# Optimization experiments

Hardware: AMD Instinct MI355X
Metric: run time of the kernel (lower is better)

## Reference

```python
import jax, jax.numpy as jnp
import numpy as np

B, D, C = 4096, 4096, 1024


def setup_inputs() -> dict:
    key = jax.random.key(0)
    kx, kw = jax.random.split(key)
    x = jax.random.normal(kx, (B, D), dtype=jnp.float32)
    # kaiming_normal_ with nonlinearity='relu': std = sqrt(2 / fan_in)
    W = jax.random.normal(kw, (C, D), dtype=jnp.float32) * jnp.sqrt(2.0 / D)
    return {"x": x, "W": W}


def reference(x, W):
    # Original: -( (x[:, :, None] - W.T[None, :, :])**2 ).mean(axis=1)
    d = x.shape[1]
    x_sq = jnp.sum(x * x, axis=1, keepdims=True)        # [B, 1]
    w_sq = jnp.sum(W * W, axis=1)[None, :]              # [1, C]
    cross = jnp.einsum('bd,cd->bc', x, W)               # [B, C] tensor-core GEMM
    return -(x_sq - 2.0 * cross + w_sq) / d
```

## Files before the change

kernel.cpp:

```cpp
#include <hip/hip_runtime.h>
#include <hip/hip_bf16.h>


typedef float f32x4 __attribute__((ext_vector_type(4)));
typedef float f32x2 __attribute__((ext_vector_type(2)));
typedef float f32x16 __attribute__((ext_vector_type(16)));
typedef int i32x4 __attribute__((ext_vector_type(4)));
typedef int i32x8 __attribute__((ext_vector_type(8)));

#define BDIM 4096
#define DDIM 4096
#define CDIM 1024
#define TM 256
#define TN 256
#define BK 64
#define KSPLIT 4
#define NIT ((DDIM / KSPLIT) / BK)
#define SCALE 32.0f
#define INV_SS (1.0f/1024.0f)
#define PSCALE 0.0625f

#define WAITV(N) asm volatile("s_waitcnt vmcnt(" #N ")" ::: "memory")

__global__ __launch_bounds__(256) void cvt_rowsq(
    const float* __restrict__ x, const float* __restrict__ W,
    unsigned char* __restrict__ xb, unsigned char* __restrict__ wb,
    float* __restrict__ xsq, float* __restrict__ wsq)
{
    const int lane = threadIdx.x & 63;
    const int row = blockIdx.x * 4 + (threadIdx.x >> 6);

    const float* src;
    unsigned char* dst;
    float* sq;
    if (row < BDIM) {
        src = x + (size_t)row * DDIM;
        dst = xb + (size_t)row * DDIM;
        sq = xsq + row;
    } else {
        int r = row - BDIM;
        src = W + (size_t)r * DDIM;
        dst = wb + (size_t)r * DDIM;
        sq = wsq + r;
    }

    const float4* s4 = (const float4*)src;
    unsigned int* d4 = (unsigned int*)dst;
    float a = 0.f;
    #pragma unroll
    for (int s = 0; s < DDIM / 4 / 64; ++s) {
        float4 f = s4[lane + 64 * s];
        a += f.x * f.x + f.y * f.y + f.z * f.z + f.w * f.w;
        unsigned int p = 0;
        p = __builtin_amdgcn_cvt_pk_fp8_f32(f.x * SCALE, f.y * SCALE, p, false);
        p = __builtin_amdgcn_cvt_pk_fp8_f32(f.z * SCALE, f.w * SCALE, p, true);
        d4[lane + 64 * s] = p;
    }
    #pragma unroll
    for (int off = 32; off > 0; off >>= 1) a += __shfl_down(a, off);
    if (lane == 0) *sq = a;
}


__device__ __forceinline__ i32x8 cat8(i32x4 lo, i32x4 hi) {
    return __builtin_shufflevector(lo, hi, 0, 1, 2, 3, 4, 5, 6, 7);
}

#define MXMFMA(A, Bv, C)                                                  \
    __builtin_amdgcn_mfma_scale_f32_32x32x64_f8f6f4(                      \
        (A), (Bv), (C), 0, 0, 0, 0x7F7F7F7F, 0, 0x7F7F7F7F)

#define GLOAD16(gp, lp)                                                   \
    __builtin_amdgcn_global_load_lds(                                     \
        (const __attribute__((address_space(1))) void*)(gp),              \
        (__attribute__((address_space(3))) void*)(lp), 16, 0, 0)

__global__ __launch_bounds__(512, 2) void gemm_eucl(
    const unsigned char* __restrict__ xb,
    const unsigned char* __restrict__ wb,
    unsigned int* __restrict__ part)
{
    __shared__ unsigned char sm[2 * 32768];

    const int tid = threadIdx.x;
    const int lane = tid & 63;
    const int w = tid >> 6;
    const int wr = w >> 2;
    const int wc = w & 3;
    const int bm = blockIdx.x * TM;
    const int bn = blockIdx.y * TN;
    const int ks = blockIdx.z * (DDIM / KSPLIT);

    const int srow = w * 32 + (lane >> 2);
    const int schunk = ((lane & 3) ^ ((lane >> 3) & 3)) * 16;
    const unsigned char* gA0 = xb + (size_t)(bm + srow) * DDIM + ks + schunk;
    const unsigned char* gA1 = gA0 + (size_t)16 * DDIM;
    const unsigned char* gB0 = wb + (size_t)(bn + srow) * DDIM + ks + schunk;
    const unsigned char* gB1 = gB0 + (size_t)16 * DDIM;
    unsigned char* lA0 = sm + w * 2048;
    unsigned char* lA1 = lA0 + 1024;
    unsigned char* lB0 = sm + 16384 + w * 2048;
    unsigned char* lB1 = lB0 + 1024;

#define STAGE_A(buf, t)                                                   \
    do {                                                                  \
        GLOAD16(gA0 + (t) * BK, lA0 + (buf) * 32768);                     \
        GLOAD16(gA1 + (t) * BK, lA1 + (buf) * 32768);                     \
    } while (0)
#define STAGE_B(buf, t)                                                   \
    do {                                                                  \
        GLOAD16(gB0 + (t) * BK, lB0 + (buf) * 32768);                     \
        GLOAD16(gB1 + (t) * BK, lB1 + (buf) * 32768);                     \
    } while (0)

    const int s_rd = ((lane & 31) >> 1) & 3;
    const int c0s = ((lane >> 5) * 2) ^ s_rd;
    const unsigned char* aR0 = sm + (wr * 128 + (lane & 31)) * 64 + c0s * 16;
    const unsigned char* aR1 = sm + (wr * 128 + (lane & 31)) * 64 + (c0s ^ 1) * 16;
    const unsigned char* bR0 = sm + 16384 + (wc * 64 + (lane & 31)) * 64 + c0s * 16;
    const unsigned char* bR1 = sm + 16384 + (wc * 64 + (lane & 31)) * 64 + (c0s ^ 1) * 16;

    f32x16 acc[8] = {};

    STAGE_B(0, 0);
    STAGE_A(0, 0);
    WAITV(0);
    __builtin_amdgcn_s_barrier();

    i32x8 fb0, fb1;

    #pragma unroll
    for (int t = 0; t < NIT; ++t) {
        const int p = t & 1;
        const int po = p * 32768;
        if (t + 1 < NIT) STAGE_B(p ^ 1, t + 1);
        fb0 = cat8(*(const i32x4*)(bR0 + po), *(const i32x4*)(bR1 + po));
        fb1 = cat8(*(const i32x4*)(bR0 + po + 2048), *(const i32x4*)(bR1 + po + 2048));
        if (t + 1 < NIT) WAITV(2);
        else             WAITV(0);
        __builtin_amdgcn_s_barrier();
        if (t + 1 < NIT) STAGE_A(p ^ 1, t + 1);
        {
            i32x8 fa0 = cat8(*(const i32x4*)(aR0 + po), *(const i32x4*)(aR1 + po));
            i32x8 fa1 = cat8(*(const i32x4*)(aR0 + po + 2048), *(const i32x4*)(aR1 + po + 2048));
            i32x8 fa2 = cat8(*(const i32x4*)(aR0 + po + 4096), *(const i32x4*)(aR1 + po + 4096));
            i32x8 fa3 = cat8(*(const i32x4*)(aR0 + po + 6144), *(const i32x4*)(aR1 + po + 6144));
            __builtin_amdgcn_s_setprio(1);
            acc[0] = MXMFMA(fa0, fb0, acc[0]);
            acc[1] = MXMFMA(fa0, fb1, acc[1]);
            acc[2] = MXMFMA(fa1, fb0, acc[2]);
            acc[3] = MXMFMA(fa1, fb1, acc[3]);
            acc[4] = MXMFMA(fa2, fb0, acc[4]);
            acc[5] = MXMFMA(fa2, fb1, acc[5]);
            acc[6] = MXMFMA(fa3, fb0, acc[6]);
            acc[7] = MXMFMA(fa3, fb1, acc[7]);
            __builtin_amdgcn_s_setprio(0);
        }
        if (t + 1 < NIT) {
            WAITV(2);
            __builtin_amdgcn_s_barrier();
        }
    }

    const int bb = blockIdx.x * 4 + blockIdx.y;
    unsigned int* p = part + ((size_t)blockIdx.z * 64 + bb) * (32 * 512);
    #pragma unroll
    for (int f = 0; f < 8; ++f)
        #pragma unroll
        for (int g = 0; g < 4; ++g) {
            unsigned int pk = 0;
            pk = __builtin_amdgcn_cvt_pk_fp8_f32(
                acc[f][g * 4 + 0] * PSCALE, acc[f][g * 4 + 1] * PSCALE, pk, false);
            pk = __builtin_amdgcn_cvt_pk_fp8_f32(
                acc[f][g * 4 + 2] * PSCALE, acc[f][g * 4 + 3] * PSCALE, pk, true);
            p[(f * 4 + g) * 512 + tid] = pk;
        }
#undef STAGE_A
#undef STAGE_B
}

__global__ __launch_bounds__(256) void reduce_out(
    const unsigned int* __restrict__ part, const float* __restrict__ xsq,
    const float* __restrict__ wsq, float* __restrict__ out)
{
    const int bid = blockIdx.x;
    const int bb = bid >> 3;
    const int w = bid & 7;
    const int wr = w >> 2, wc = w & 3;
    const int t = threadIdx.x;
    const int lane = t & 63;
    const int g = t >> 6;
    const int bm = (bb >> 2) * TM, bn = (bb & 3) * TN;
    const size_t sl = (size_t)64 * 32 * 512;
    const float c1 = 2.0f * 16.0f * INV_SS / (float)DDIM;
    const float c2 = 1.0f / (float)DDIM;

    #pragma unroll
    for (int f = 0; f < 8; ++f) {
        size_t o = ((size_t)bb * 32 + f * 4 + g) * 512 + w * 64 + lane;
        f32x2 s01 = {0.f, 0.f}, s23 = {0.f, 0.f};
        #pragma unroll
        for (int z = 0; z < KSPLIT; ++z) {
            unsigned int u = part[o + (size_t)z * sl];
            s01 += __builtin_amdgcn_cvt_pk_f32_fp8(u, false);
            s23 += __builtin_amdgcn_cvt_pk_f32_fp8(u, true);
        }
        int i = f >> 1, j = f & 1;
        int gn = bn + wc * 64 + j * 32 + (lane & 31);
        float wv = wsq[gn];
        int gm0 = bm + wr * 128 + i * 32 + 8 * g + 4 * (lane >> 5);
        float sv[4] = {s01.x, s01.y, s23.x, s23.y};
        #pragma unroll
        for (int r = 0; r < 4; ++r) {
            out[(size_t)(gm0 + r) * CDIM + gn] = sv[r] * c1 - (xsq[gm0 + r] + wv) * c2;
        }
    }
}

__global__ void fallback_kernel(const float* __restrict__ x, const float* __restrict__ W,
                                float* __restrict__ out)
{
    int c = blockIdx.x * blockDim.x + threadIdx.x;
    int b = blockIdx.y;
    if (c >= CDIM) return;
    const float* xr = x + (size_t)b * DDIM;
    const float* wr = W + (size_t)c * DDIM;
    float xs = 0.f, ws = 0.f, cr = 0.f;
    for (int d = 0; d < DDIM; ++d) {
        float xv = xr[d], wv = wr[d];
        xs += xv * xv; ws += wv * wv; cr += xv * wv;
    }
    out[(size_t)b * CDIM + c] = (2.0f * cr - xs - ws) / (float)DDIM;
}

extern "C" void kernel_launch(void* const* d_in, const int* in_sizes, int n_in,
                              void* d_out, int out_size, void* d_ws, size_t ws_size,
                              hipStream_t stream) {
    const float* x = (const float*)d_in[0];
    const float* W = (const float*)d_in[1];
    float* out = (float*)d_out;

    size_t need = (size_t)(BDIM + CDIM) * DDIM
                + (size_t)(BDIM + CDIM) * sizeof(float)
                + (size_t)KSPLIT * BDIM * CDIM;
    if (ws_size < need) {
        fallback_kernel<<<dim3(CDIM / 256, BDIM), 256, 0, stream>>>(x, W, out);
        return;
    }

    unsigned char* xb = (unsigned char*)d_ws;
    unsigned char* wb = xb + (size_t)BDIM * DDIM;
    float* xsq = (float*)(wb + (size_t)CDIM * DDIM);
    float* wsq = xsq + BDIM;
    unsigned int* part = (unsigned int*)(wsq + CDIM);

    cvt_rowsq<<<(BDIM + CDIM) / 4, 256, 0, stream>>>(x, W, xb, wb, xsq, wsq);
    gemm_eucl<<<dim3(BDIM / TM, CDIM / TN, KSPLIT), 512, 0, stream>>>(xb, wb, part);
    reduce_out<<<512, 256, 0, stream>>>(part, xsq, wsq, out);
}
```

Measured before the change: 135.4 us.

## Triple-buffer LDS tiles and prefetch two stages ahead with one barrier

```diff
diff --git a/kernel.cpp b/kernel.cpp
--- a/kernel.cpp
+++ b/kernel.cpp
@@ -80,7 +80,7 @@
     const unsigned char* __restrict__ wb,
     unsigned int* __restrict__ part)
 {
-    __shared__ unsigned char sm[2 * 32768];
+    __shared__ unsigned char sm[3 * 32768];
 
     const int tid = threadIdx.x;
     const int lane = tid & 63;
@@ -102,15 +102,12 @@
     unsigned char* lB0 = sm + 16384 + w * 2048;
     unsigned char* lB1 = lB0 + 1024;
 
-#define STAGE_A(buf, t)                                                   \
+#define STAGE(q, t)                                                       \
     do {                                                                  \
-        GLOAD16(gA0 + (t) * BK, lA0 + (buf) * 32768);                     \
-        GLOAD16(gA1 + (t) * BK, lA1 + (buf) * 32768);                     \
-    } while (0)
-#define STAGE_B(buf, t)                                                   \
-    do {                                                                  \
-        GLOAD16(gB0 + (t) * BK, lB0 + (buf) * 32768);                     \
-        GLOAD16(gB1 + (t) * BK, lB1 + (buf) * 32768);                     \
+        GLOAD16(gA0 + (t) * BK, lA0 + (q) * 32768);                       \
+        GLOAD16(gA1 + (t) * BK, lA1 + (q) * 32768);                       \
+        GLOAD16(gB0 + (t) * BK, lB0 + (q) * 32768);                       \
+        GLOAD16(gB1 + (t) * BK, lB1 + (q) * 32768);                       \
     } while (0)
 
     const int s_rd = ((lane & 31) >> 1) & 3;
@@ -122,44 +119,36 @@
 
     f32x16 acc[8] = {};
 
-    STAGE_B(0, 0);
-    STAGE_A(0, 0);
-    WAITV(0);
-    __builtin_amdgcn_s_barrier();
-
-    i32x8 fb0, fb1;
+    STAGE(0, 0);
+    STAGE(1, 1);
 
     #pragma unroll
     for (int t = 0; t < NIT; ++t) {
-        const int p = t & 1;
-        const int po = p * 32768;
-        if (t + 1 < NIT) STAGE_B(p ^ 1, t + 1);
-        fb0 = cat8(*(const i32x4*)(bR0 + po), *(const i32x4*)(bR1 + po));
-        fb1 = cat8(*(const i32x4*)(bR0 + po + 2048), *(const i32x4*)(bR1 + po + 2048));
-        if (t + 1 < NIT) WAITV(2);
+        const int qo = (t % 3) * 32768;
+        if (t + 1 < NIT) WAITV(4);
         else             WAITV(0);
         __builtin_amdgcn_s_barrier();
-        if (t + 1 < NIT) STAGE_A(p ^ 1, t + 1);
-        {
-            i32x8 fa0 = cat8(*(const i32x4*)(aR0 + po), *(const i32x4*)(aR1 + po));
-            i32x8 fa1 = cat8(*(const i32x4*)(aR0 + po + 2048), *(const i32x4*)(aR1 + po + 2048));
-            i32x8 fa2 = cat8(*(const i32x4*)(aR0 + po + 4096), *(const i32x4*)(aR1 + po + 4096));
-            i32x8 fa3 = cat8(*(const i32x4*)(aR0 + po + 6144), *(const i32x4*)(aR1 + po + 6144));
-            __builtin_amdgcn_s_setprio(1);
-            acc[0] = MXMFMA(fa0, fb0, acc[0]);
-            acc[1] = MXMFMA(fa0, fb1, acc[1]);
-            acc[2] = MXMFMA(fa1, fb0, acc[2]);
-            acc[3] = MXMFMA(fa1, fb1, acc[3]);
-            acc[4] = MXMFMA(fa2, fb0, acc[4]);
-            acc[5] = MXMFMA(fa2, fb1, acc[5]);
-            acc[6] = MXMFMA(fa3, fb0, acc[6]);
-            acc[7] = MXMFMA(fa3, fb1, acc[7]);
-            __builtin_amdgcn_s_setprio(0);
-        }
-        if (t + 1 < NIT) {
-            WAITV(2);
-            __builtin_amdgcn_s_barrier();
-        }
+        if (t + 2 < NIT) STAGE((t + 2) % 3, t + 2);
+        i32x8 fb0 = cat8(*(const i32x4*)(bR0 + qo), *(const i32x4*)(bR1 + qo));
+        i32x8 fb1 = cat8(*(const i32x4*)(bR0 + qo + 2048),
+                         *(const i32x4*)(bR1 + qo + 2048));
+        i32x8 fa0 = cat8(*(const i32x4*)(aR0 + qo), *(const i32x4*)(aR1 + qo));
+        i32x8 fa1 = cat8(*(const i32x4*)(aR0 + qo + 2048),
+                         *(const i32x4*)(aR1 + qo + 2048));
+        i32x8 fa2 = cat8(*(const i32x4*)(aR0 + qo + 4096),
+                         *(const i32x4*)(aR1 + qo + 4096));
+        i32x8 fa3 = cat8(*(const i32x4*)(aR0 + qo + 6144),
+                         *(const i32x4*)(aR1 + qo + 6144));
+        __builtin_amdgcn_s_setprio(1);
+        acc[0] = MXMFMA(fa0, fb0, acc[0]);
+        acc[1] = MXMFMA(fa0, fb1, acc[1]);
+        acc[2] = MXMFMA(fa1, fb0, acc[2]);
+        acc[3] = MXMFMA(fa1, fb1, acc[3]);
+        acc[4] = MXMFMA(fa2, fb0, acc[4]);
+        acc[5] = MXMFMA(fa2, fb1, acc[5]);
+        acc[6] = MXMFMA(fa3, fb0, acc[6]);
+        acc[7] = MXMFMA(fa3, fb1, acc[7]);
+        __builtin_amdgcn_s_setprio(0);
     }
 
     const int bb = blockIdx.x * 4 + blockIdx.y;
@@ -175,8 +164,7 @@
                 acc[f][g * 4 + 2] * PSCALE, acc[f][g * 4 + 3] * PSCALE, pk, true);
             p[(f * 4 + g) * 512 + tid] = pk;
         }
-#undef STAGE_A
-#undef STAGE_B
+#undef STAGE
 }
 
 __global__ __launch_bounds__(256) void reduce_out(
```

Measured after the change: 135.6 us. No clear change (+0.2%).
